# Performance work log

Hardware: AMD Instinct MI355X
Metric: run time of the kernel (lower is better)

The kernel has to match this reference:

```python
import jax, jax.numpy as jnp
import numpy as np

HEADS = 8
DIM_HEAD = 64
SCALE = DIM_HEAD ** -0.5


def setup_inputs() -> dict:
    key = jax.random.key(0)
    k1, k2, k3 = jax.random.split(key, 3)
    b, dim, n = 4, 256, 2048
    hidden = HEADS * DIM_HEAD  # 512
    x = jax.random.normal(k1, (b, dim, n), dtype=jnp.float32)
    # Conv1d kernel-size-1 weights are pointwise linear maps over channels.
    w_qkv = jax.random.normal(k2, (3 * hidden, dim), dtype=jnp.float32) * (dim ** -0.5)
    w_out = jax.random.normal(k3, (dim, hidden), dtype=jnp.float32) * (hidden ** -0.5)
    b_out = jnp.zeros((dim,), dtype=jnp.float32)
    return {"x": x, "w_qkv": w_qkv, "w_out": w_out, "b_out": b_out}


def reference(x, w_qkv, w_out, b_out):
    b, dim, n = x.shape
    hidden = w_out.shape[1]
    # pointwise conv1d == channel matmul: [3h, dim] x [b, dim, n] -> [b, 3h, n]
    qkv = jnp.einsum('oi,bin->bon', w_qkv, x)
    q, k, v = jnp.split(qkv, 3, axis=1)
    # b (h c) n -> b h c n
    reshape = lambda t: t.reshape(b, HEADS, DIM_HEAD, n)
    q, k, v = reshape(q) * SCALE, reshape(k), reshape(v)
    sim = jnp.einsum('bhdi,bhdj->bhij', q, k)          # [b, h, n, n]
    attn = jax.nn.softmax(sim, axis=-1)
    out = jnp.einsum('bhij,bhdj->bhid', attn, v)        # [b, h, n, d]
    # b h n d -> b (h d) n
    out = out.transpose(0, 1, 3, 2).reshape(b, hidden, n)
    return jnp.einsum('oi,bin->bon', w_out, out) + b_out[None, :, None]
```

## Files before the change

### kernel.cpp

```cpp
#include <hip/hip_runtime.h>
#include <stdint.h>

#define SEQ  2048
#define DIMC 256
#define HID  512
#define NH   8
#define DH   64

typedef __attribute__((ext_vector_type(8))) short bf16x8;
typedef __attribute__((ext_vector_type(4))) float f32x4;
typedef __attribute__((ext_vector_type(16))) float f32x16;
typedef __attribute__((ext_vector_type(2))) unsigned uint2v;
typedef __attribute__((address_space(1))) const uint32_t guint_t;
typedef __attribute__((address_space(3))) uint32_t luint_t;

__device__ __forceinline__ void gld16(const void* g, void* l) {
  __builtin_amdgcn_global_load_lds((guint_t*)g, (luint_t*)l, 16, 0, 0);
}

__device__ __forceinline__ uint32_t fbits(float f) {
  union { float f; uint32_t u; } v; v.f = f; return v.u;
}
__device__ __forceinline__ unsigned short f2bf(float f) {
  uint32_t u = fbits(f);
  return (unsigned short)((u + 0x7FFFu + ((u >> 16) & 1u)) >> 16);
}
__device__ __forceinline__ uint32_t pku(uint32_t u0, uint32_t u1) {
  return __builtin_amdgcn_perm(u1 + 0x8000u, u0 + 0x8000u, 0x07060302u);
}

__device__ __forceinline__ void swap32(uint32_t& a, uint32_t& b) {
#if __has_builtin(__builtin_amdgcn_permlane32_swap)
  uint2v r = __builtin_amdgcn_permlane32_swap(a, b, false, false);
  a = r[0]; b = r[1];
#else
  uint32_t aw = __shfl_xor(a, 32);
  uint32_t bw = __shfl_xor(b, 32);
  bool lo = (threadIdx.x & 32) == 0;
  uint32_t an = lo ? a : bw;
  uint32_t bn = lo ? aw : b;
  a = an; b = bn;
#endif
}

__global__ __launch_bounds__(256) void prep_kernel(
    const float* __restrict__ x, const float* __restrict__ wqkv,
    const float* __restrict__ wout,
    unsigned short* __restrict__ wqkv_b, unsigned short* __restrict__ wout_b,
    unsigned short* __restrict__ xT) {
  __shared__ float tile[64][65];
  int blk = blockIdx.x;
  int t = threadIdx.x;
  if (blk < 384) {
    int idx = blk * 1024 + t * 4;
    float4 v = *(const float4*)(wqkv + idx);
    float s = ((idx >> 8) < HID) ? 0.18033688011112042f : 1.0f;
    ushort4 o;
    o.x = f2bf(v.x * s); o.y = f2bf(v.y * s);
    o.z = f2bf(v.z * s); o.w = f2bf(v.w * s);
    *(ushort4*)(wqkv_b + idx) = o;
    return;
  }
  if (blk < 512) {
    int idx = (blk - 384) * 1024 + t * 4;
    float4 v = *(const float4*)(wout + idx);
    ushort4 o;
    o.x = f2bf(v.x); o.y = f2bf(v.y); o.z = f2bf(v.z); o.w = f2bf(v.w);
    *(ushort4*)(wout_b + idx) = o;
    return;
  }
  int tid = blk - 512;
  int b  = tid >> 7;
  int r  = tid & 127;
  int i0 = (r >> 5) * 64;
  int n0 = (r & 31) * 64;
  const float* xb = x + (size_t)b * DIMC * SEQ;
  int tn = t & 15, ti = t >> 4;
#pragma unroll
  for (int j = 0; j < 4; j++) {
    int il = ti + j * 16;
    float4 v = *(const float4*)(xb + (size_t)(i0 + il) * SEQ + n0 + tn * 4);
    tile[il][tn*4+0] = v.x; tile[il][tn*4+1] = v.y;
    tile[il][tn*4+2] = v.z; tile[il][tn*4+3] = v.w;
  }
  __syncthreads();
  unsigned short* xTb = xT + (size_t)b * SEQ * DIMC;
#pragma unroll
  for (int j = 0; j < 4; j++) {
    int nl = ti + j * 16;
    int i4 = tn * 4;
    uint2 pk;
    pk.x = (uint32_t)f2bf(tile[i4+0][nl]) | ((uint32_t)f2bf(tile[i4+1][nl]) << 16);
    pk.y = (uint32_t)f2bf(tile[i4+2][nl]) | ((uint32_t)f2bf(tile[i4+3][nl]) << 16);
    *(uint2*)(xTb + (size_t)(n0 + nl) * DIMC + i0 + i4) = pk;
  }
}

__global__ __launch_bounds__(256, 2) void qkv_gemm(
    const unsigned short* __restrict__ wq, const unsigned short* __restrict__ xT,
    unsigned short* __restrict__ Qs, unsigned short* __restrict__ Ks,
    unsigned short* __restrict__ Vt) {
  __shared__ unsigned short lds[17408];
  unsigned short* la = lds;
  unsigned short* lb = lds + 8192;
  int o0 = blockIdx.x * 128;
  int n0 = blockIdx.y * 128;
  int b  = blockIdx.z;
  int t  = threadIdx.x;
  int wv = t >> 6, l = t & 63, l15 = l & 15, q = l >> 4;
  int wm = (wv & 1) * 64, wn = (wv >> 1) * 64;
  f32x4 acc[4][4];
#pragma unroll
  for (int i = 0; i < 4; i++)
#pragma unroll
    for (int j = 0; j < 4; j++) acc[i][j] = (f32x4){0.f, 0.f, 0.f, 0.f};
  const unsigned short* Ag = wq + (size_t)o0 * DIMC;
  const unsigned short* Bg = xT + ((size_t)b * SEQ + n0) * DIMC;
  int lrow8 = l >> 3, lcol = l & 7;
  for (int kk = 0; kk < 4; kk++) {
    int k0 = kk * 64;
    __syncthreads();
#pragma unroll
    for (int c0 = 0; c0 < 4; c0++) {
      int c = wv * 4 + c0;
      int row = c * 8 + lrow8;
      int sg = lcol ^ (row & 7);
      gld16(Ag + (size_t)row * DIMC + k0 + sg * 8, la + c * 512);
      gld16(Bg + (size_t)row * DIMC + k0 + sg * 8, lb + c * 512);
    }
    __syncthreads();
#pragma unroll
    for (int kh = 0; kh < 2; kh++) {
      bf16x8 af[4], bfr[4];
#pragma unroll
      for (int mt = 0; mt < 4; mt++) {
        int row = wm + mt*16 + l15;
        af[mt] = *(const bf16x8*)(la + row*64 + ((kh*4 + q) ^ (row & 7)) * 8);
      }
#pragma unroll
      for (int nt = 0; nt < 4; nt++) {
        int row = wn + nt*16 + l15;
        bfr[nt] = *(const bf16x8*)(lb + row*64 + ((kh*4 + q) ^ (row & 7)) * 8);
      }
#pragma unroll
      for (int mt = 0; mt < 4; mt++)
#pragma unroll
        for (int nt = 0; nt < 4; nt++)
          acc[mt][nt] = __builtin_amdgcn_mfma_f32_16x16x32_bf16(af[mt], bfr[nt], acc[mt][nt], 0, 0, 0);
    }
  }
  __syncthreads();
  int seg3 = o0 >> 9;
  int h0   = (o0 & 511) >> 6;
  if (seg3 == 2) {
#pragma unroll
    for (int mt = 0; mt < 4; mt++)
#pragma unroll
      for (int nt = 0; nt < 4; nt++)
#pragma unroll
        for (int r = 0; r < 4; r++) {
          int ol = wm + mt * 16 + q * 4 + r;
          int h = h0 + (ol >> 6), d = ol & 63;
          int n = n0 + wn + nt * 16 + l15;
          Vt[(((size_t)b * NH + h) * DH + d) * SEQ + n] = f2bf(acc[mt][nt][r]);
        }
  } else {
    unsigned short* dst = (seg3 == 0) ? Qs : Ks;
#pragma unroll
    for (int mt = 0; mt < 4; mt++)
#pragma unroll
      for (int nt = 0; nt < 4; nt++)
#pragma unroll
        for (int r = 0; r < 4; r++) {
          int ol = wm + mt * 16 + q * 4 + r;
          int nn = wn + nt * 16 + l15;
          lds[nn * 136 + ol] = f2bf(acc[mt][nt][r]);
        }
    __syncthreads();
#pragma unroll
    for (int i = 0; i < 8; i++) {
      int idx = i * 256 + t;
      int nn  = idx >> 4;
      int olb = (idx & 15) * 8;
      uint4 v = *(const uint4*)(lds + nn * 136 + olb);
      int h = h0 + (olb >> 6), d = olb & 63;
      *(uint4*)(dst + (((size_t)b * NH + h) * SEQ + n0 + nn) * DH + d) = v;
    }
  }
}

__global__ __launch_bounds__(256, 2) void attn_kernel(
    const unsigned short* __restrict__ Qs, const unsigned short* __restrict__ Ks,
    const unsigned short* __restrict__ Vt, unsigned short* __restrict__ AO) {
  __shared__ float Ocf[8192];
  __shared__ float Lc[256];
  int n0 = blockIdx.x * 64;
  int bh = blockIdx.y;
  int b = bh >> 3, h = bh & 7;
  int t = threadIdx.x;
  int cg = t >> 6, l = t & 63, l31 = l & 31, lh = l >> 5;
  const unsigned short* Qg = Qs + ((size_t)bh * SEQ + n0) * DH;
  bf16x8 qb[2][4];
#pragma unroll
  for (int qt = 0; qt < 2; qt++)
#pragma unroll
    for (int kc = 0; kc < 4; kc++)
      qb[qt][kc] = *(const bf16x8*)(Qg + (qt*32 + l31) * DH + kc*16 + lh*8);
  f32x16 oacc[2][2];
  float lrowp[2] = {0.f, 0.f};
#pragma unroll
  for (int qt = 0; qt < 2; qt++)
#pragma unroll
    for (int dt = 0; dt < 2; dt++)
#pragma unroll
      for (int r = 0; r < 16; r++) oacc[qt][dt][r] = 0.f;
  const unsigned short* Kg = Ks + ((size_t)bh * SEQ + cg * 512) * DH;
  const unsigned short* Vg = Vt + (size_t)bh * DH * SEQ + cg * 512;
  for (int it = 0; it < 16; it++) {
    int kb = it * 32;
    bf16x8 vf[2][2];
#pragma unroll
    for (int kc2 = 0; kc2 < 2; kc2++)
#pragma unroll
      for (int dt = 0; dt < 2; dt++)
        vf[kc2][dt] = *(const bf16x8*)(Vg + (size_t)(dt*32 + l31) * SEQ + kb + kc2*16 + lh*8);
    f32x16 st[2];
#pragma unroll
    for (int qt = 0; qt < 2; qt++)
#pragma unroll
      for (int r = 0; r < 16; r++) st[qt][r] = 0.f;
#pragma unroll
    for (int kc = 0; kc < 4; kc++) {
      bf16x8 kf = *(const bf16x8*)(Kg + (size_t)(kb + l31) * DH + kc*16 + lh*8);
      st[0] = __builtin_amdgcn_mfma_f32_32x32x16_bf16(kf, qb[0][kc], st[0], 0, 0, 0);
      st[1] = __builtin_amdgcn_mfma_f32_32x32x16_bf16(kf, qb[1][kc], st[1], 0, 0, 0);
    }
#pragma unroll
    for (int qt = 0; qt < 2; qt++) {
      float p[16];
      float s0 = 0.f;
#pragma unroll
      for (int r = 0; r < 16; r++) { p[r] = __builtin_amdgcn_exp2f(st[qt][r]); s0 += p[r]; }
      lrowp[qt] += s0;
      bf16x8 af[2];
#pragma unroll
      for (int hf = 0; hf < 2; hf++) {
        uint32_t xs[4], ys[4];
#pragma unroll
        for (int j = 0; j < 4; j++) {
          xs[j] = fbits(p[hf*8 + j]);
          ys[j] = fbits(p[hf*8 + 4 + j]);
          swap32(xs[j], ys[j]);
        }
        union { uint32_t u[4]; bf16x8 v; } cv;
        cv.u[0] = pku(xs[0], xs[1]);
        cv.u[1] = pku(xs[2], xs[3]);
        cv.u[2] = pku(ys[0], ys[1]);
        cv.u[3] = pku(ys[2], ys[3]);
        af[hf] = cv.v;
      }
#pragma unroll
      for (int kc2 = 0; kc2 < 2; kc2++)
#pragma unroll
        for (int dt = 0; dt < 2; dt++)
          oacc[qt][dt] = __builtin_amdgcn_mfma_f32_32x32x16_bf16(af[kc2], vf[kc2][dt], oacc[qt][dt], 0, 0, 0);
    }
  }
#pragma unroll
  for (int qt = 0; qt < 2; qt++) {
    float v = lrowp[qt];
    v += __shfl_xor(v, 32);
    if (l < 32) Lc[cg * 64 + qt * 32 + l31] = v;
  }
  auto dump = [&](float* R) {
#pragma unroll
    for (int qt = 0; qt < 2; qt++)
#pragma unroll
      for (int dt = 0; dt < 2; dt++)
#pragma unroll
        for (int rr = 0; rr < 4; rr++)
          *(f32x4*)(R + ((qt*2+dt)*4 + rr) * 256 + l * 4) =
            (f32x4){oacc[qt][dt][rr*4+0], oacc[qt][dt][rr*4+1],
                    oacc[qt][dt][rr*4+2], oacc[qt][dt][rr*4+3]};
  };
  auto addin = [&](const float* R) {
#pragma unroll
    for (int qt = 0; qt < 2; qt++)
#pragma unroll
      for (int dt = 0; dt < 2; dt++)
#pragma unroll
        for (int rr = 0; rr < 4; rr++) {
          f32x4 v = *(const f32x4*)(R + ((qt*2+dt)*4 + rr) * 256 + l * 4);
          oacc[qt][dt][rr*4+0] += v[0]; oacc[qt][dt][rr*4+1] += v[1];
          oacc[qt][dt][rr*4+2] += v[2]; oacc[qt][dt][rr*4+3] += v[3];
        }
  };
  if (cg == 1) dump(Ocf);
  if (cg == 3) dump(Ocf + 4096);
  __syncthreads();
  if (cg == 0) addin(Ocf);
  if (cg == 2) addin(Ocf + 4096);
  __syncthreads();
  if (cg == 2) dump(Ocf);
  __syncthreads();
  if (cg == 0) {
    addin(Ocf);
    unsigned short* AOb = AO + (size_t)b * SEQ * HID + h * DH;
#pragma unroll
    for (int qt = 0; qt < 2; qt++)
#pragma unroll
      for (int r = 0; r < 16; r++) {
        int qrow = qt*32 + (r & 3) + 8*(r >> 2) + 4*lh;
        float lsum = Lc[qrow] + Lc[64 + qrow] + Lc[128 + qrow] + Lc[192 + qrow];
        float inv = __builtin_amdgcn_rcpf(lsum);
        int n = n0 + qrow;
#pragma unroll
        for (int dt = 0; dt < 2; dt++)
          AOb[(size_t)n * HID + dt*32 + l31] = f2bf(oacc[qt][dt][r] * inv);
      }
  }
}

__global__ __launch_bounds__(256, 2) void out_gemm(
    const unsigned short* __restrict__ wo, const unsigned short* __restrict__ AO,
    const float* __restrict__ bias, float* __restrict__ out) {
  __shared__ unsigned short la[64 * 64];
  __shared__ unsigned short lb[128 * 64];
  int o0 = blockIdx.x * 64;
  int n0 = blockIdx.y * 128;
  int b  = blockIdx.z;
  int t  = threadIdx.x;
  int wv = t >> 6, l = t & 63, l15 = l & 15, q = l >> 4;
  int wm = (wv & 1) * 32, wn = (wv >> 1) * 64;
  f32x4 acc[2][4];
#pragma unroll
  for (int i = 0; i < 2; i++)
#pragma unroll
    for (int j = 0; j < 4; j++) acc[i][j] = (f32x4){0.f,0.f,0.f,0.f};
  const unsigned short* Ag = wo + (size_t)o0 * HID;
  const unsigned short* Bg = AO + ((size_t)b * SEQ + n0) * HID;
  int lrow8 = l >> 3, lcol = l & 7;
  for (int kk = 0; kk < 8; kk++) {
    int k0 = kk * 64;
    __syncthreads();
#pragma unroll
    for (int c0 = 0; c0 < 2; c0++) {
      int c = wv * 2 + c0;
      int row = c * 8 + lrow8;
      int sg = lcol ^ (row & 7);
      gld16(Ag + (size_t)row * HID + k0 + sg * 8, la + c * 512);
    }
#pragma unroll
    for (int c0 = 0; c0 < 4; c0++) {
      int c = wv * 4 + c0;
      int row = c * 8 + lrow8;
      int sg = lcol ^ (row & 7);
      gld16(Bg + (size_t)row * HID + k0 + sg * 8, lb + c * 512);
    }
    __syncthreads();
#pragma unroll
    for (int kh = 0; kh < 2; kh++) {
      bf16x8 af[2], bfr[4];
#pragma unroll
      for (int mt = 0; mt < 2; mt++) {
        int row = wm + mt*16 + l15;
        af[mt] = *(const bf16x8*)(la + row*64 + ((kh*4 + q) ^ (row & 7)) * 8);
      }
#pragma unroll
      for (int nt = 0; nt < 4; nt++) {
        int row = wn + nt*16 + l15;
        bfr[nt] = *(const bf16x8*)(lb + row*64 + ((kh*4 + q) ^ (row & 7)) * 8);
      }
#pragma unroll
      for (int mt = 0; mt < 2; mt++)
#pragma unroll
        for (int nt = 0; nt < 4; nt++)
          acc[mt][nt] = __builtin_amdgcn_mfma_f32_16x16x32_bf16(af[mt], bfr[nt], acc[mt][nt], 0,0,0);
    }
  }
#pragma unroll
  for (int mt = 0; mt < 2; mt++)
#pragma unroll
    for (int nt = 0; nt < 4; nt++)
#pragma unroll
      for (int r = 0; r < 4; r++) {
        int o2 = o0 + wm + mt*16 + q*4 + r;
        int n  = n0 + wn + nt*16 + l15;
        out[((size_t)b * DIMC + o2) * SEQ + n] = acc[mt][nt][r] + bias[o2];
      }
}

extern "C" void kernel_launch(void* const* d_in, const int* in_sizes, int n_in,
                              void* d_out, int out_size, void* d_ws, size_t ws_size,
                              hipStream_t stream) {
  const float* x    = (const float*)d_in[0];
  const float* wqkv = (const float*)d_in[1];
  const float* wout = (const float*)d_in[2];
  const float* bout = (const float*)d_in[3];
  float* out = (float*)d_out;
  char* ws = (char*)d_ws;
  unsigned short* wqkv_b = (unsigned short*)(ws);
  unsigned short* wout_b = (unsigned short*)(ws + 786432);
  unsigned short* xT     = (unsigned short*)(ws + 1048576);
  unsigned short* Qs     = (unsigned short*)(ws + 5242880);
  unsigned short* Ks     = (unsigned short*)(ws + 13631488);
  unsigned short* Vt     = (unsigned short*)(ws + 22020096);
  unsigned short* AO     = (unsigned short*)(ws + 30408704);
  prep_kernel<<<1024, 256, 0, stream>>>(x, wqkv, wout, wqkv_b, wout_b, xT);
  qkv_gemm<<<dim3(12, 16, 4), 256, 0, stream>>>(wqkv_b, xT, Qs, Ks, Vt);
  attn_kernel<<<dim3(32, 32), 256, 0, stream>>>(Qs, Ks, Vt, AO);
  out_gemm<<<dim3(4, 16, 4), 256, 0, stream>>>(wout_b, AO, bout, out);
}
```

Before: 154.8 us.

## Stage K/V tiles through swizzled LDS in attention; shrink out_gemm M tile

In the attention kernel each wave now copies its K and V chunk into a per-wave LDS region with global_load_lds and an XOR swizzle, then reads MFMA fragments from LDS. This replaces the strided direct global fragment loads, which on V read rows SEQ apart. The old float O-reduction buffer is replaced by a bf16 K/V buffer that is reused as the float reduction buffer after a barrier, so LDS use stays the same. Separately, out_gemm's M tile drops from 64 to 32 and the grid doubles, trading per-block reuse for more blocks in flight.

```diff
diff --git a/kernel.cpp b/kernel.cpp
--- a/kernel.cpp
+++ b/kernel.cpp
@@ -192,7 +192,7 @@
 __global__ __launch_bounds__(256, 2) void attn_kernel(
     const unsigned short* __restrict__ Qs, const unsigned short* __restrict__ Ks,
     const unsigned short* __restrict__ Vt, unsigned short* __restrict__ AO) {
-  __shared__ float Ocf[8192];
+  __shared__ unsigned short KV[16384];
   __shared__ float Lc[256];
   int n0 = blockIdx.x * 64;
   int bh = blockIdx.y;
@@ -216,14 +216,22 @@
       for (int r = 0; r < 16; r++) oacc[qt][dt][r] = 0.f;
   const unsigned short* Kg = Ks + ((size_t)bh * SEQ + cg * 512) * DH;
   const unsigned short* Vg = Vt + (size_t)bh * DH * SEQ + cg * 512;
+  unsigned short* Kw = KV + cg * 4096;
+  unsigned short* Vw = Kw + 2048;
   for (int it = 0; it < 16; it++) {
     int kb = it * 32;
-    bf16x8 vf[2][2];
-#pragma unroll
-    for (int kc2 = 0; kc2 < 2; kc2++)
-#pragma unroll
-      for (int dt = 0; dt < 2; dt++)
-        vf[kc2][dt] = *(const bf16x8*)(Vg + (size_t)(dt*32 + l31) * SEQ + kb + kc2*16 + lh*8);
+#pragma unroll
+    for (int g = 0; g < 4; g++) {
+      int kr = g * 8 + (l >> 3);
+      gld16(Kg + (size_t)(kb + kr) * DH + ((l & 7) ^ (kr & 7)) * 8, Kw + g * 512);
+    }
+#pragma unroll
+    for (int g = 0; g < 4; g++) {
+      int dr = g * 16 + (l >> 2);
+      int seg = (l & 3) ^ ((dr ^ (dr >> 2)) & 3);
+      gld16(Vg + (size_t)dr * SEQ + kb + seg * 8, Vw + g * 512);
+    }
+    __builtin_amdgcn_s_waitcnt(0x0F70);
     f32x16 st[2];
 #pragma unroll
     for (int qt = 0; qt < 2; qt++)
@@ -231,10 +239,19 @@
       for (int r = 0; r < 16; r++) st[qt][r] = 0.f;
 #pragma unroll
     for (int kc = 0; kc < 4; kc++) {
-      bf16x8 kf = *(const bf16x8*)(Kg + (size_t)(kb + l31) * DH + kc*16 + lh*8);
+      bf16x8 kf = *(const bf16x8*)(Kw + l31 * 64 + (((kc*2 + lh) ^ (l31 & 7))) * 8);
       st[0] = __builtin_amdgcn_mfma_f32_32x32x16_bf16(kf, qb[0][kc], st[0], 0, 0, 0);
       st[1] = __builtin_amdgcn_mfma_f32_32x32x16_bf16(kf, qb[1][kc], st[1], 0, 0, 0);
     }
+    bf16x8 vf[2][2];
+#pragma unroll
+    for (int kc2 = 0; kc2 < 2; kc2++)
+#pragma unroll
+      for (int dt = 0; dt < 2; dt++) {
+        int d = dt*32 + l31;
+        int hv = (d ^ (d >> 2)) & 3;
+        vf[kc2][dt] = *(const bf16x8*)(Vw + d * 32 + (((kc2*2 + lh) ^ hv)) * 8);
+      }
 #pragma unroll
     for (int qt = 0; qt < 2; qt++) {
       float p[16];
@@ -272,6 +289,8 @@
     v += __shfl_xor(v, 32);
     if (l < 32) Lc[cg * 64 + qt * 32 + l31] = v;
   }
+  __syncthreads();
+  float* Ocf = (float*)KV;
   auto dump = [&](float* R) {
 #pragma unroll
     for (int qt = 0; qt < 2; qt++)
@@ -324,31 +343,27 @@
 __global__ __launch_bounds__(256, 2) void out_gemm(
     const unsigned short* __restrict__ wo, const unsigned short* __restrict__ AO,
     const float* __restrict__ bias, float* __restrict__ out) {
-  __shared__ unsigned short la[64 * 64];
+  __shared__ unsigned short la[32 * 64];
   __shared__ unsigned short lb[128 * 64];
-  int o0 = blockIdx.x * 64;
+  int o0 = blockIdx.x * 32;
   int n0 = blockIdx.y * 128;
   int b  = blockIdx.z;
   int t  = threadIdx.x;
   int wv = t >> 6, l = t & 63, l15 = l & 15, q = l >> 4;
-  int wm = (wv & 1) * 32, wn = (wv >> 1) * 64;
-  f32x4 acc[2][4];
-#pragma unroll
-  for (int i = 0; i < 2; i++)
-#pragma unroll
-    for (int j = 0; j < 4; j++) acc[i][j] = (f32x4){0.f,0.f,0.f,0.f};
+  int wm = (wv & 1) * 16, wn = (wv >> 1) * 64;
+  f32x4 acc[4];
+#pragma unroll
+  for (int j = 0; j < 4; j++) acc[j] = (f32x4){0.f,0.f,0.f,0.f};
   const unsigned short* Ag = wo + (size_t)o0 * HID;
   const unsigned short* Bg = AO + ((size_t)b * SEQ + n0) * HID;
   int lrow8 = l >> 3, lcol = l & 7;
   for (int kk = 0; kk < 8; kk++) {
     int k0 = kk * 64;
     __syncthreads();
-#pragma unroll
-    for (int c0 = 0; c0 < 2; c0++) {
-      int c = wv * 2 + c0;
-      int row = c * 8 + lrow8;
+    {
+      int row = wv * 8 + lrow8;
       int sg = lcol ^ (row & 7);
-      gld16(Ag + (size_t)row * HID + k0 + sg * 8, la + c * 512);
+      gld16(Ag + (size_t)row * HID + k0 + sg * 8, la + wv * 512);
     }
 #pragma unroll
     for (int c0 = 0; c0 < 4; c0++) {
@@ -360,11 +375,10 @@
     __syncthreads();
 #pragma unroll
     for (int kh = 0; kh < 2; kh++) {
-      bf16x8 af[2], bfr[4];
-#pragma unroll
-      for (int mt = 0; mt < 2; mt++) {
-        int row = wm + mt*16 + l15;
-        af[mt] = *(const bf16x8*)(la + row*64 + ((kh*4 + q) ^ (row & 7)) * 8);
+      bf16x8 af, bfr[4];
+      {
+        int row = wm + l15;
+        af = *(const bf16x8*)(la + row*64 + ((kh*4 + q) ^ (row & 7)) * 8);
       }
 #pragma unroll
       for (int nt = 0; nt < 4; nt++) {
@@ -372,22 +386,18 @@
         bfr[nt] = *(const bf16x8*)(lb + row*64 + ((kh*4 + q) ^ (row & 7)) * 8);
       }
 #pragma unroll
-      for (int mt = 0; mt < 2; mt++)
-#pragma unroll
-        for (int nt = 0; nt < 4; nt++)
-          acc[mt][nt] = __builtin_amdgcn_mfma_f32_16x16x32_bf16(af[mt], bfr[nt], acc[mt][nt], 0,0,0);
-    }
-  }
-#pragma unroll
-  for (int mt = 0; mt < 2; mt++)
-#pragma unroll
-    for (int nt = 0; nt < 4; nt++)
-#pragma unroll
-      for (int r = 0; r < 4; r++) {
-        int o2 = o0 + wm + mt*16 + q*4 + r;
-        int n  = n0 + wn + nt*16 + l15;
-        out[((size_t)b * DIMC + o2) * SEQ + n] = acc[mt][nt][r] + bias[o2];
-      }
+      for (int nt = 0; nt < 4; nt++)
+        acc[nt] = __builtin_amdgcn_mfma_f32_16x16x32_bf16(af, bfr[nt], acc[nt], 0,0,0);
+    }
+  }
+#pragma unroll
+  for (int nt = 0; nt < 4; nt++)
+#pragma unroll
+    for (int r = 0; r < 4; r++) {
+      int o2 = o0 + wm + q*4 + r;
+      int n  = n0 + wn + nt*16 + l15;
+      out[((size_t)b * DIMC + o2) * SEQ + n] = acc[nt][r] + bias[o2];
+    }
 }
 
 extern "C" void kernel_launch(void* const* d_in, const int* in_sizes, int n_in,
@@ -409,5 +419,5 @@
   prep_kernel<<<1024, 256, 0, stream>>>(x, wqkv, wout, wqkv_b, wout_b, xT);
   qkv_gemm<<<dim3(12, 16, 4), 256, 0, stream>>>(wqkv_b, xT, Qs, Ks, Vt);
   attn_kernel<<<dim3(32, 32), 256, 0, stream>>>(Qs, Ks, Vt, AO);
-  out_gemm<<<dim3(4, 16, 4), 256, 0, stream>>>(wout_b, AO, bout, out);
-}
+  out_gemm<<<dim3(8, 16, 4), 256, 0, stream>>>(wout_b, AO, bout, out);
+}
```

Result: faster. 145.4 us (-6.0%).
